# Performance work log

Measured on AMD Instinct MI355X. Metric: run time of the kernel, lower is better.

The kernel has to match this reference:

```python
import jax, jax.numpy as jnp
import numpy as np

B, SX, SY, D = 32, 2048, 2048, 160

def setup_inputs() -> dict:
    key = jax.random.key(0)
    ks = jax.random.split(key, 5)
    s = 1.0 / np.sqrt(D)
    return {
        "x": jax.random.normal(ks[0], (B, SX, D), dtype=jnp.float32),
        "y": jax.random.normal(ks[1], (B, SY, D), dtype=jnp.float32),
        "Wq": jax.random.normal(ks[2], (D, D), dtype=jnp.float32) * s,
        "bq": jnp.zeros((D,), dtype=jnp.float32),
        "Wk": jax.random.normal(ks[3], (D, D), dtype=jnp.float32) * s,
        "bk": jnp.zeros((D,), dtype=jnp.float32),
        "Wv": jax.random.normal(ks[4], (D, D), dtype=jnp.float32) * s,
        "bv": jnp.zeros((D,), dtype=jnp.float32),
    }

def reference(x, y, Wq, bq, Wk, bk, Wv, bv):
    # torch nn.Linear: out = in @ W.T + b, W is [out_dim, in_dim]
    q = jnp.einsum('bxd,ed->bxe', x, Wq) + bq          # [B,SX,D]
    k = jnp.einsum('byd,ed->bye', y, Wk) + bk          # [B,SY,D]
    v = jnp.einsum('byd,ed->bye', y, Wv) + bv          # [B,SY,D]
    scores = jnp.einsum('bxd,byd->bxy', q, k)          # [B,SX,SY] (no scaling in source)
    attn = jax.nn.softmax(scores, axis=-1)
    out = jnp.einsum('bxy,byd->bxd', attn, v)          # dropout is identity at eval
    return out + x                                     # residual
```

## Files before the change

### kernel.cpp

```cpp
#include <hip/hip_runtime.h>

#define LOG2E 1.44269504088896340736f

typedef _Float16 f16;
typedef __attribute__((ext_vector_type(2))) _Float16 f16x2;
typedef __attribute__((ext_vector_type(2))) __fp16 fp16x2;
typedef __attribute__((ext_vector_type(4))) _Float16 f16x4;
typedef __attribute__((ext_vector_type(8))) _Float16 f16x8;
typedef __attribute__((ext_vector_type(4))) float f32x4;
typedef __attribute__((ext_vector_type(16))) float f32x16;
typedef __attribute__((ext_vector_type(8))) unsigned short us8;
typedef __attribute__((ext_vector_type(2))) int i32x2;

#define BB 32
#define SSX 2048
#define SSY 2048
#define DD 160
#define M_TOTAL (BB*SSX)

#define PRS 168
#define VTRS 136
#define RS 168

__device__ __forceinline__ f32x4 mfma16(f16x8 a, f16x8 b, f32x4 c) {
  return __builtin_amdgcn_mfma_f32_16x16x32_f16(a, b, c, 0, 0, 0);
}

__device__ __forceinline__ f32x16 mfma32(f16x8 a, f16x8 b, f32x16 c) {
  return __builtin_amdgcn_mfma_f32_32x32x16_f16(a, b, c, 0, 0, 0);
}

__device__ __forceinline__ unsigned pk2rtz(float a, float b) {
  union { fp16x2 h; unsigned u; } x;
  x.h = __builtin_amdgcn_cvt_pkrtz(a, b);
  return x.u;
}

__global__ __launch_bounds__(256) void wcvt_kernel(
    const float* __restrict__ Wq, const float* __restrict__ Wk, const float* __restrict__ Wv,
    f16* __restrict__ Wf)
{
  int idx = blockIdx.x*256 + threadIdx.x;
  int which = idx / 6400;
  int off   = idx % 6400;
  const float* src = (which == 0) ? Wq : (which == 1 ? Wk : Wv);
  float4 v = *(const float4*)&src[off*4];
  f16x4 h = { (f16)v.x, (f16)v.y, (f16)v.z, (f16)v.w };
  *(f16x4*)&Wf[which*25600 + off*4] = h;
}

__global__ __launch_bounds__(256, 3) void proj_kernel(
    const float* __restrict__ x, const float* __restrict__ y,
    const float* __restrict__ bq, const float* __restrict__ bk, const float* __restrict__ bv,
    const f16* __restrict__ Wf,
    f16* __restrict__ Qw, f16* __restrict__ Kw, f16* __restrict__ Vtw)
{
  __shared__ __align__(16) f16 buf[160*PRS];
  const int t = threadIdx.x;
  const int wave = t >> 6;
  const int lane = t & 63;
  const int quad = lane >> 4;
  const int l16  = lane & 15;
  const int bid  = (blockIdx.x & 7) * 128 + (blockIdx.x >> 3);
  const int kind = bid & 1;
  const int tile = bid >> 1;
  const int row0 = tile * 128;
  const float* src = kind ? y : x;

  for (int i = 0; i < 20; ++i) {
    int idx = t + i*256;
    int r = idx / 40, c4 = idx % 40;
    float4 v = *(const float4*)&src[(size_t)(row0 + r)*DD + c4*4];
    f16x4 h = { (f16)v.x, (f16)v.y, (f16)v.z, (f16)v.w };
    *(f16x4*)&buf[r*PRS + c4*4] = h;
  }
  __syncthreads();
  f16x8 afr0[5], afr1[5];
  #pragma unroll
  for (int ks = 0; ks < 5; ++ks) {
    afr0[ks] = *(const f16x8*)&buf[(wave*32 + l16)*PRS + ks*32 + quad*8];
    afr1[ks] = *(const f16x8*)&buf[(wave*32 + 16 + l16)*PRS + ks*32 + quad*8];
  }
  __syncthreads();

#define LOAD_W(mat) { \
  for (int i = 0; i < 13; ++i) { \
    int idx = t + i*256; \
    if (idx < 3200) { \
      int r = idx / 20, g = idx % 20; \
      *(us8*)&buf[r*PRS + g*8] = *(const us8*)&Wf[(mat)*25600 + r*160 + g*8]; \
    } \
  } }

#define MFMA_PASS(bias) { \
  _Pragma("unroll") \
  for (int nt = 0; nt < 10; ++nt) { \
    float bs = (bias)[nt*16 + l16]; \
    acc0[nt] = (f32x4){bs,bs,bs,bs}; \
    acc1[nt] = (f32x4){bs,bs,bs,bs}; \
    _Pragma("unroll") \
    for (int ks = 0; ks < 5; ++ks) { \
      f16x8 bfr = *(const f16x8*)&buf[(nt*16 + l16)*PRS + ks*32 + quad*8]; \
      acc0[nt] = mfma16(afr0[ks], bfr, acc0[nt]); \
      acc1[nt] = mfma16(afr1[ks], bfr, acc1[nt]); \
    } \
  } }

  f32x4 acc0[10], acc1[10];

  LOAD_W(kind ? 1 : 0);
  __syncthreads();
  MFMA_PASS(kind ? bk : bq);
  __syncthreads();
  {
    f16* dst = kind ? Kw : Qw;
    #pragma unroll
    for (int nt = 0; nt < 10; ++nt)
      #pragma unroll
      for (int r = 0; r < 4; ++r) {
        buf[(wave*32 + quad*4 + r)*PRS + nt*16 + l16]      = (f16)acc0[nt][r];
        buf[(wave*32 + 16 + quad*4 + r)*PRS + nt*16 + l16] = (f16)acc1[nt][r];
      }
    __syncthreads();
    for (int i = 0; i < 10; ++i) {
      int idx = t + i*256;
      int r = idx / 20, g = idx % 20;
      *(us8*)&dst[(size_t)(row0 + r)*DD + g*8] = *(const us8*)&buf[r*PRS + g*8];
    }
  }
  if (!kind) return;

  __syncthreads();
  LOAD_W(2);
  __syncthreads();
  MFMA_PASS(bv);
  __syncthreads();
  {
    #pragma unroll
    for (int nt = 0; nt < 10; ++nt)
      #pragma unroll
      for (int r = 0; r < 4; ++r) {
        buf[(nt*16 + l16)*VTRS + wave*32 + quad*4 + r]      = (f16)acc0[nt][r];
        buf[(nt*16 + l16)*VTRS + wave*32 + 16 + quad*4 + r] = (f16)acc1[nt][r];
      }
    __syncthreads();
    const int b  = row0 / SSY;
    const int y0 = row0 % SSY;
    for (int i = 0; i < 10; ++i) {
      int idx = t + i*256;
      int d = idx / 16, yg = idx % 16;
      *(us8*)&Vtw[((size_t)b*DD + d)*SSY + y0 + yg*8] = *(const us8*)&buf[d*VTRS + yg*8];
    }
  }
}


#define LOAD_CHUNK(yb) { \
  const f16* ksrc = Kw + ((size_t)b*SSY + (yb))*DD; \
  const f16* vsrc = Vtw + (size_t)b*DD*SSY + (yb); \
  _Pragma("unroll") \
  for (int i = 0; i < 5; ++i) { \
    int idx = t + i*256; int r = idx/20, c = idx%20; \
    kreg[i] = *(const us8*)&ksrc[(size_t)r*DD + c*8]; \
  } \
  _Pragma("unroll") \
  for (int i = 0; i < 5; ++i) { \
    int idx = t + i*256; int d = idx>>3, g = idx&7; \
    vreg[i] = *(const us8*)&vsrc[(size_t)d*SSY + g*8]; \
  } \
}

#define STORE_CHUNK() { \
  _Pragma("unroll") \
  for (int i = 0; i < 5; ++i) { \
    int idx = t + i*256; int r = idx/20, c = idx%20; \
    *(us8*)&K_lds[r*RS + c*8] = kreg[i]; \
  } \
  _Pragma("unroll") \
  for (int i = 0; i < 5; ++i) { \
    int idx = t + i*256; int d = idx>>3, g = idx&7; \
    *(us8*)&Vt_lds[d*64 + ((g ^ (d & 7)) << 3)] = vreg[i]; \
  } \
}

__global__ __launch_bounds__(256, 2) void flash_kernel(
    const f16* __restrict__ Qw, const f16* __restrict__ Kw, const f16* __restrict__ Vtw,
    const float* __restrict__ x, float* __restrict__ out)
{
  __shared__ __align__(16) f16 K_lds[64*RS];
  __shared__ __align__(16) f16 Vt_lds[160*64];
  const int t = threadIdx.x;
  const int wave = t >> 6;
  const int lane = t & 63;
  const int l31  = lane & 31;
  const int hi   = lane >> 5;
  const int bid  = (blockIdx.x & 7) * 64 + (blockIdx.x >> 3);
  const int b    = bid >> 4;
  const int x0   = (bid & 15) * 128;

  us8 kreg[5], vreg[5];
  LOAD_CHUNK(0);

  f16x8 qfr[10];
  #pragma unroll
  for (int h = 0; h < 2; ++h) {
    if (h) __syncthreads();
    const f16* qsrc = Qw + ((size_t)b*SSX + x0 + h*64)*DD;
    for (int i = 0; i < 5; ++i) {
      int idx = t + i*256;
      int r = idx / 20, c = idx % 20;
      *(us8*)&K_lds[r*RS + c*8] = *(const us8*)&qsrc[(size_t)r*DD + c*8];
    }
    __syncthreads();
    if ((wave >> 1) == h) {
      const int base = (wave & 1)*32;
      #pragma unroll
      for (int s = 0; s < 10; ++s)
        qfr[s] = *(const f16x8*)&K_lds[(base + l31)*RS + s*16 + hi*8];
    }
  }

  f32x16 acc[5];
  #pragma unroll
  for (int i = 0; i < 5; ++i)
    #pragma unroll
    for (int r = 0; r < 16; ++r) acc[i][r] = 0.f;
  float m = -1e30f, l = 0.f;

  for (int yc = 0; yc < SSY/64; ++yc) {
    __syncthreads();
    STORE_CHUNK();
    __syncthreads();
    if (yc < SSY/64 - 1) LOAD_CHUNK((yc+1)*64);

    f32x16 S0, S1;
    #pragma unroll
    for (int r = 0; r < 16; ++r) { S0[r] = 0.f; S1[r] = 0.f; }
    __builtin_amdgcn_s_setprio(1);
    #pragma unroll
    for (int s = 0; s < 10; ++s) {
      f16x8 k0 = *(const f16x8*)&K_lds[l31*RS + s*16 + hi*8];
      f16x8 k1 = *(const f16x8*)&K_lds[(32 + l31)*RS + s*16 + hi*8];
      S0 = mfma32(k0, qfr[s], S0);
      S1 = mfma32(k1, qfr[s], S1);
    }
    __builtin_amdgcn_s_setprio(0);

    float pmax = fmaxf(S0[0], S0[1]);
    #pragma unroll
    for (int r = 2; r < 16; r += 2) pmax = fmaxf(fmaxf(pmax, S0[r]), S0[r+1]);
    #pragma unroll
    for (int r = 0; r < 16; r += 2) pmax = fmaxf(fmaxf(pmax, S1[r]), S1[r+1]);
    pmax = fmaxf(pmax, __shfl_xor(pmax, 32));

    if (__any(pmax > m + 8.f)) {
      float n  = fmaxf(m, pmax);
      float sc = exp2f((m - n)*LOG2E);
      m = n; l *= sc;
      #pragma unroll
      for (int r = 0; r < 16; ++r) {
        float scq = __shfl(sc, (r&3) + 8*(r>>2) + 4*hi);
        #pragma unroll
        for (int dt = 0; dt < 5; ++dt) acc[dt][r] *= scq;
      }
    }

    float lsum = 0.f;
    #pragma unroll
    for (int r = 0; r < 16; ++r) { S0[r] = exp2f((S0[r] - m)*LOG2E); lsum += S0[r]; }
    #pragma unroll
    for (int r = 0; r < 16; ++r) { S1[r] = exp2f((S1[r] - m)*LOG2E); lsum += S1[r]; }
    lsum += __shfl_xor(lsum, 32);
    l += lsum;

    #pragma unroll
    for (int c = 0; c < 4; ++c) {
      const int bo = (c & 1)*8;
      float s0 = (c < 2) ? S0[bo+0] : S1[bo+0];
      float s1 = (c < 2) ? S0[bo+1] : S1[bo+1];
      float s2 = (c < 2) ? S0[bo+2] : S1[bo+2];
      float s3 = (c < 2) ? S0[bo+3] : S1[bo+3];
      float s4 = (c < 2) ? S0[bo+4] : S1[bo+4];
      float s5 = (c < 2) ? S0[bo+5] : S1[bo+5];
      float s6 = (c < 2) ? S0[bo+6] : S1[bo+6];
      float s7 = (c < 2) ? S0[bo+7] : S1[bo+7];
      unsigned L0 = pk2rtz(s0, s1), L1 = pk2rtz(s2, s3);
      unsigned H0 = pk2rtz(s4, s5), H1 = pk2rtz(s6, s7);
      i32x2 r02 = __builtin_amdgcn_permlane32_swap((int)L0, (int)H0, false, false);
      i32x2 r13 = __builtin_amdgcn_permlane32_swap((int)L1, (int)H1, false, false);
      union { unsigned u[4]; f16x8 h; } ph;
      ph.u[0] = (unsigned)r02.x; ph.u[1] = (unsigned)r13.x;
      ph.u[2] = (unsigned)r02.y; ph.u[3] = (unsigned)r13.y;
      __builtin_amdgcn_s_setprio(1);
      #pragma unroll
      for (int dt = 0; dt < 5; ++dt) {
        int row = dt*32 + l31;
        f16x8 vf = *(const f16x8*)&Vt_lds[row*64 + (((c*2 + hi) ^ (row & 7)) << 3)];
        acc[dt] = mfma32(ph.h, vf, acc[dt]);
      }
      __builtin_amdgcn_s_setprio(0);
    }
  }

  #pragma unroll
  for (int r = 0; r < 16; ++r) {
    int qr = (r&3) + 8*(r>>2) + 4*hi;
    float rl = 1.f / __shfl(l, qr);
    size_t rowoff = ((size_t)b*SSX + x0 + wave*32 + qr)*DD + l31;
    #pragma unroll
    for (int dt = 0; dt < 5; ++dt) {
      size_t o = rowoff + (size_t)dt*32;
      out[o] = acc[dt][r]*rl + x[o];
    }
  }
}

extern "C" void kernel_launch(void* const* d_in, const int* in_sizes, int n_in,
                              void* d_out, int out_size, void* d_ws, size_t ws_size,
                              hipStream_t stream) {
  const float* x  = (const float*)d_in[0];
  const float* y  = (const float*)d_in[1];
  const float* Wq = (const float*)d_in[2];
  const float* bq = (const float*)d_in[3];
  const float* Wk = (const float*)d_in[4];
  const float* bk = (const float*)d_in[5];
  const float* Wv = (const float*)d_in[6];
  const float* bv = (const float*)d_in[7];

  f16* Qw  = (f16*)d_ws;
  f16* Kw  = Qw + (size_t)M_TOTAL*DD;
  f16* Vtw = Kw + (size_t)M_TOTAL*DD;
  size_t wf_off = (ws_size - 153600) & ~(size_t)255;
  f16* Wf = (f16*)((char*)d_ws + wf_off);

  wcvt_kernel<<<75, 256, 0, stream>>>(Wq, Wk, Wv, Wf);
  proj_kernel<<<1024, 256, 0, stream>>>(x, y, bq, bk, bv, Wf, Qw, Kw, Vtw);
  flash_kernel<<<512, 256, 0, stream>>>(Qw, Kw, Vtw, x, (float*)d_out);
}
```

Baseline: 290.3 us.

## Split projection into separate Q/K/V blocks, load fragments directly from global

The projection kernel now launches three block kinds per 128-row tile (Q, K, V) instead of two, where the y-tile blocks previously computed both K and V serially. Input fragments are loaded straight from global fp32 and converted in registers, and weight fragments are read from the fp16 global copy instead of being staged in LDS. This removes several barriers and LDS staging passes and balances work across blocks. In exchange, y is read twice from memory and weight reads rely on cache hits.

```diff
diff --git a/kernel.cpp b/kernel.cpp
--- a/kernel.cpp
+++ b/kernel.cpp
@@ -55,65 +55,53 @@
     const f16* __restrict__ Wf,
     f16* __restrict__ Qw, f16* __restrict__ Kw, f16* __restrict__ Vtw)
 {
-  __shared__ __align__(16) f16 buf[160*PRS];
+  __shared__ __align__(16) f16 buf[160*VTRS];
   const int t = threadIdx.x;
   const int wave = t >> 6;
   const int lane = t & 63;
   const int quad = lane >> 4;
   const int l16  = lane & 15;
-  const int bid  = (blockIdx.x & 7) * 128 + (blockIdx.x >> 3);
-  const int kind = bid & 1;
-  const int tile = bid >> 1;
+  const int bid  = (blockIdx.x & 7) * 192 + (blockIdx.x >> 3);
+  const int kind = bid % 3;
+  const int tile = bid / 3;
   const int row0 = tile * 128;
-  const float* src = kind ? y : x;
-
-  for (int i = 0; i < 20; ++i) {
-    int idx = t + i*256;
-    int r = idx / 40, c4 = idx % 40;
-    float4 v = *(const float4*)&src[(size_t)(row0 + r)*DD + c4*4];
-    f16x4 h = { (f16)v.x, (f16)v.y, (f16)v.z, (f16)v.w };
-    *(f16x4*)&buf[r*PRS + c4*4] = h;
-  }
-  __syncthreads();
+  const float* src  = (kind == 0) ? x  : y;
+  const f16*   W    = Wf + kind*25600;
+  const float* bias = (kind == 0) ? bq : (kind == 1 ? bk : bv);
+
   f16x8 afr0[5], afr1[5];
+  {
+    const float* r0p = src + (size_t)(row0 + wave*32 + l16)*DD;
+    const float* r1p = r0p + 16*DD;
+    #pragma unroll
+    for (int ks = 0; ks < 5; ++ks) {
+      float4 a = *(const float4*)&r0p[ks*32 + quad*8];
+      float4 b = *(const float4*)&r0p[ks*32 + quad*8 + 4];
+      afr0[ks] = (f16x8){(f16)a.x,(f16)a.y,(f16)a.z,(f16)a.w,
+                         (f16)b.x,(f16)b.y,(f16)b.z,(f16)b.w};
+      float4 c = *(const float4*)&r1p[ks*32 + quad*8];
+      float4 d = *(const float4*)&r1p[ks*32 + quad*8 + 4];
+      afr1[ks] = (f16x8){(f16)c.x,(f16)c.y,(f16)c.z,(f16)c.w,
+                         (f16)d.x,(f16)d.y,(f16)d.z,(f16)d.w};
+    }
+  }
+
+  f32x4 acc0[10], acc1[10];
   #pragma unroll
-  for (int ks = 0; ks < 5; ++ks) {
-    afr0[ks] = *(const f16x8*)&buf[(wave*32 + l16)*PRS + ks*32 + quad*8];
-    afr1[ks] = *(const f16x8*)&buf[(wave*32 + 16 + l16)*PRS + ks*32 + quad*8];
-  }
-  __syncthreads();
-
-#define LOAD_W(mat) { \
-  for (int i = 0; i < 13; ++i) { \
-    int idx = t + i*256; \
-    if (idx < 3200) { \
-      int r = idx / 20, g = idx % 20; \
-      *(us8*)&buf[r*PRS + g*8] = *(const us8*)&Wf[(mat)*25600 + r*160 + g*8]; \
-    } \
-  } }
-
-#define MFMA_PASS(bias) { \
-  _Pragma("unroll") \
-  for (int nt = 0; nt < 10; ++nt) { \
-    float bs = (bias)[nt*16 + l16]; \
-    acc0[nt] = (f32x4){bs,bs,bs,bs}; \
-    acc1[nt] = (f32x4){bs,bs,bs,bs}; \
-    _Pragma("unroll") \
-    for (int ks = 0; ks < 5; ++ks) { \
-      f16x8 bfr = *(const f16x8*)&buf[(nt*16 + l16)*PRS + ks*32 + quad*8]; \
-      acc0[nt] = mfma16(afr0[ks], bfr, acc0[nt]); \
-      acc1[nt] = mfma16(afr1[ks], bfr, acc1[nt]); \
-    } \
-  } }
-
-  f32x4 acc0[10], acc1[10];
-
-  LOAD_W(kind ? 1 : 0);
-  __syncthreads();
-  MFMA_PASS(kind ? bk : bq);
-  __syncthreads();
-  {
-    f16* dst = kind ? Kw : Qw;
+  for (int nt = 0; nt < 10; ++nt) {
+    float bs = bias[nt*16 + l16];
+    acc0[nt] = (f32x4){bs,bs,bs,bs};
+    acc1[nt] = (f32x4){bs,bs,bs,bs};
+    #pragma unroll
+    for (int ks = 0; ks < 5; ++ks) {
+      f16x8 bfr = *(const f16x8*)&W[(nt*16 + l16)*160 + ks*32 + quad*8];
+      acc0[nt] = mfma16(afr0[ks], bfr, acc0[nt]);
+      acc1[nt] = mfma16(afr1[ks], bfr, acc1[nt]);
+    }
+  }
+
+  if (kind < 2) {
+    f16* dst = (kind == 0) ? Qw : Kw;
     #pragma unroll
     for (int nt = 0; nt < 10; ++nt)
       #pragma unroll
@@ -127,15 +115,7 @@
       int r = idx / 20, g = idx % 20;
       *(us8*)&dst[(size_t)(row0 + r)*DD + g*8] = *(const us8*)&buf[r*PRS + g*8];
     }
-  }
-  if (!kind) return;
-
-  __syncthreads();
-  LOAD_W(2);
-  __syncthreads();
-  MFMA_PASS(bv);
-  __syncthreads();
-  {
+  } else {
     #pragma unroll
     for (int nt = 0; nt < 10; ++nt)
       #pragma unroll
@@ -334,6 +314,6 @@
   f16* Wf = (f16*)((char*)d_ws + wf_off);
 
   wcvt_kernel<<<75, 256, 0, stream>>>(Wq, Wk, Wv, Wf);
-  proj_kernel<<<1024, 256, 0, stream>>>(x, y, bq, bk, bv, Wf, Qw, Kw, Vtw);
+  proj_kernel<<<1536, 256, 0, stream>>>(x, y, bq, bk, bv, Wf, Qw, Kw, Vtw);
   flash_kernel<<<512, 256, 0, stream>>>(Qw, Kw, Vtw, x, (float*)d_out);
 }
```

New measurement: 291.1 us. Within noise of the previous version (+0.3%).
